# Kernel tuning notes

Hardware: AMD Instinct MI355X
Metric: run time of the kernel (lower is better)

## Reference

```python
import jax, jax.numpy as jnp
import numpy as np

B, N, F_IN, H = 16, 2048, 6, 64
NEG_INF = -jnp.inf


def setup_inputs() -> dict:
    key = jax.random.key(0)
    ks = jax.random.split(key, 16)
    x = jax.random.normal(ks[0], (B, N, F_IN), dtype=jnp.float32)
    adj = jax.random.bernoulli(ks[1], 0.5, (B, N, N)).astype(jnp.int32)
    valid = int(N * 0.9)
    mask = jnp.broadcast_to((jnp.arange(N) < valid).astype(jnp.float32)[None, :, None], (B, N, 1))
    mask = jnp.array(mask)

    def lin(k, fi, fo):
        return jax.random.normal(k, (fi, fo), dtype=jnp.float32) / np.sqrt(fi)

    return {
        'x': x, 'adj': adj, 'mask': mask,
        'W1': lin(ks[2], F_IN, H), 'a_src1': lin(ks[3], H, 1), 'a_dst1': lin(ks[4], H, 1),
        'W2': lin(ks[5], H, H), 'a_src2': lin(ks[6], H, 1), 'a_dst2': lin(ks[7], H, 1),
        'actor_w1': lin(ks[8], H, 32), 'actor_b1': jnp.zeros((32,), jnp.float32),
        'actor_w2': lin(ks[9], 32, 1), 'actor_b2': jnp.zeros((1,), jnp.float32),
        'critic_w1': lin(ks[10], H, 32), 'critic_b1': jnp.zeros((32,), jnp.float32),
        'critic_w2': lin(ks[11], 32, 1), 'critic_b2': jnp.zeros((1,), jnp.float32),
    }


def gat_layer(x, adj, mask, W, a_src, a_dst):
    h = x @ W                                    # [B,N,H]
    s = h @ a_src                                # [B,N,1]
    d = h @ a_dst                                # [B,N,1]
    e = jax.nn.leaky_relu(s + jnp.swapaxes(d, -1, -2), 0.2)   # [B,N,N]
    e = jnp.where(adj == 0, NEG_INF, e)
    e = jnp.where(jnp.swapaxes(mask, -1, -2) == 0, NEG_INF, e)
    alpha = jnp.nan_to_num(jax.nn.softmax(e, axis=-1))
    out = alpha @ h + h
    return jax.nn.elu(out) * mask


def reference(x, adj, mask, W1, a_src1, a_dst1, W2, a_src2, a_dst2,
              actor_w1, actor_b1, actor_w2, actor_b2,
              critic_w1, critic_b1, critic_w2, critic_b2):
    h = gat_layer(x, adj, mask, W1, a_src1, a_dst1)
    h = gat_layer(h, adj, mask, W2, a_src2, a_dst2)
    logits = (jax.nn.elu(h @ actor_w1 + actor_b1) @ actor_w2 + actor_b2)[..., 0]  # [B,N]
    sum_h = h.sum(axis=1)                                   # [B,H]
    valid_counts = jnp.clip(mask.sum(axis=1), 1.0)          # [B,1]
    global_h = sum_h / valid_counts
    value = (jax.nn.elu(global_h @ critic_w1 + critic_b1) @ critic_w2 + critic_b2)[..., 0]  # [B]
    return logits, value
```

## Files before the change

kernel.cpp:

```cpp
#include <hip/hip_runtime.h>
#include <hip/hip_bf16.h>

constexpr int kB = 16;
constexpr int kN = 2048;
constexpr int kH = 64;
constexpr int kF = 6;

typedef short s16x8 __attribute__((ext_vector_type(8)));
typedef float f32x4 __attribute__((ext_vector_type(4)));

__device__ __forceinline__ unsigned short f2bf(float f) {
  __hip_bfloat16 h = __float2bfloat16(f);
  unsigned short u;
  __builtin_memcpy(&u, &h, 2);
  return u;
}

__device__ __forceinline__ float bf2f(unsigned short u) {
  unsigned int b = ((unsigned int)u) << 16;
  float f;
  __builtin_memcpy(&f, &b, 4);
  return f;
}

__device__ __forceinline__ float eluf(float x) {
  return x > 0.0f ? x : __expf(x) - 1.0f;
}

__device__ __forceinline__ unsigned int pack8(uint4 a, uint4 b) {
  unsigned int t1 = (a.y << 1) + a.x;
  unsigned int t2 = (a.w << 1) + a.z;
  unsigned int n0 = (t2 << 2) + t1;
  unsigned int u1 = (b.y << 1) + b.x;
  unsigned int u2 = (b.w << 1) + b.z;
  unsigned int n1 = (u2 << 2) + u1;
  return (n1 << 4) + n0;
}

__global__ __launch_bounds__(256) void k_embed(
    const float* __restrict__ x, const float* __restrict__ W,
    const float* __restrict__ asrc, const float* __restrict__ adst,
    const float* __restrict__ mask,
    float* __restrict__ hf, unsigned short* __restrict__ hT,
    unsigned int* __restrict__ uvpk, float* __restrict__ Rr,
    float* __restrict__ sumh,
    const float* __restrict__ W2,
    unsigned short* __restrict__ w2thi, unsigned short* __restrict__ w2tlo) {
  __shared__ float lh[64][65];
  __shared__ float psd[2][4][64];
  const int r0 = blockIdx.x * 64;
  const int b = r0 >> 11;
  const int i0 = r0 & (kN - 1);
  const int t = threadIdx.x;
  const int k = t & 63;
  const int w = t >> 6;
  if (blockIdx.x == 0) {
#pragma unroll
    for (int i = 0; i < 4; ++i) sumh[t + 256 * i] = 0.0f;
  }
  if (blockIdx.x == 1) {
#pragma unroll
    for (int i = 0; i < 16; ++i) {
      const int idx = t + 256 * i;
      const int col = idx & 63, kk = idx >> 6;
      const float wv = W2[kk * kH + col];
      const unsigned short hh = f2bf(wv);
      w2thi[col * 64 + kk] = hh;
      w2tlo[col * 64 + kk] = f2bf(wv - bf2f(hh));
    }
  }
  for (int it = 0; it < 16; ++it) {
    const int rl = w * 16 + it;
    const int row = r0 + rl;
    float h = 0.0f;
#pragma unroll
    for (int f = 0; f < kF; ++f) h = fmaf(x[(size_t)row * kF + f], W[f * kH + k], h);
    lh[rl][k] = h;
    hf[(size_t)row * kH + k] = h;
  }
  __syncthreads();
  float sp = 0.0f, dp = 0.0f;
#pragma unroll
  for (int kk = 0; kk < 16; ++kk) {
    const int k2 = w * 16 + kk;
    const float hv = lh[k][k2];
    sp = fmaf(hv, asrc[k2], sp);
    dp = fmaf(hv, adst[k2], dp);
  }
  psd[0][w][k] = sp;
  psd[1][w][k] = dp;
  __syncthreads();
  if (t < 64) {
    const float s = psd[0][0][t] + psd[0][1][t] + psd[0][2][t] + psd[0][3][t];
    const float d = psd[1][0][t] + psd[1][1][t] + psd[1][2][t] + psd[1][3][t];
    const int row = r0 + t;
    const bool mv = mask[row] != 0.0f;
    const float u = mv ? __expf(d) : 0.0f;
    const float v = mv ? __expf(0.2f * d) : 0.0f;
    uvpk[row] = ((unsigned int)f2bf(u) << 16) | f2bf(v);
    Rr[row] = __expf(-0.8f * s);
  }
  const size_t tb = (size_t)b * kN * kH + (size_t)(i0 >> 5) * 2048;
  for (int it = 0; it < 16; ++it) {
    const int kk = w * 16 + it;
    hT[tb + (size_t)(k >> 5) * 2048 + kk * 32 + (k & 31)] = f2bf(lh[k][kk]);
  }
}

template <bool PACK, bool TAIL, bool EMB>
__global__ __launch_bounds__(256) void k_attn(
    const int* __restrict__ adj, unsigned int* __restrict__ bits,
    const unsigned short* __restrict__ hT,
    const unsigned int* __restrict__ uvpk, const float* __restrict__ Rr,
    const float* __restrict__ hres, const float* __restrict__ mask,
    const float* __restrict__ aw1, const float* __restrict__ ab1,
    const float* __restrict__ aw2, const float* __restrict__ ab2,
    float* __restrict__ logits, float* __restrict__ sumh,
    const unsigned short* __restrict__ w2thi, const unsigned short* __restrict__ w2tlo,
    const float* __restrict__ asrc2, const float* __restrict__ adst2,
    float* __restrict__ h2res, unsigned short* __restrict__ hT2,
    unsigned int* __restrict__ uv2, float* __restrict__ Rr2) {
  __shared__ __align__(16) char smem[32896];
  unsigned int* uvl = (unsigned int*)smem;
  unsigned int* blw = (unsigned int*)(smem + 8192);
  unsigned short* hbase = (unsigned short*)(smem + 16512);

  const int bid0 = blockIdx.x;
  const int swz = (bid0 & 7) * 128 + (bid0 >> 3);
  const int b = swz >> 6;
  const int rb = swz & 63;
  const int row0 = rb * 32;

  const int t = threadIdx.x;
  const int wv = t >> 6;
  const int l = t & 63;
  const int r = l & 15;
  const int g = l >> 4;
  const int rt = wv & 1;
  const int hf2 = wv >> 1;
  const int rloc = rt * 16 + r;

  {
    const uint4* src = (const uint4*)(uvpk + (size_t)b * kN);
    ((uint4*)uvl)[t] = src[t];
    ((uint4*)uvl)[t + 256] = src[t + 256];
  }

  const unsigned short* hTb = hT + (size_t)b * kN * kH;
  {
    *(uint4*)(hbase + 0 * 2048 + t * 8) = *(const uint4*)(hTb + t * 8);
    *(uint4*)(hbase + 1 * 2048 + t * 8) = *(const uint4*)(hTb + (size_t)32 * 2048 + t * 8);
  }
  uint4 hc0 = *(const uint4*)(hTb + (size_t)1 * 2048 + t * 8);
  uint4 hc1 = *(const uint4*)(hTb + (size_t)33 * 2048 + t * 8);
  uint4 hn0 = {}, hn1 = {};

  const int brow = t >> 3;
  const int bc = t & 7;
  const int bh = bc >> 2;
  const int bq4 = bc & 3;
  const int* adjL = adj + ((size_t)b * kN + row0 + brow) * kN + bh * 1024 + bq4 * 8;
  uint4 qcA = {}, qcB = {}, qnA = {}, qnB = {};
  if (PACK) {
    const uint4 a0 = *(const uint4*)(adjL);
    const uint4 a1 = *(const uint4*)(adjL + 4);
    ((unsigned char*)blw)[(brow * 65 + bh * 32) * 4 + bq4] = (unsigned char)pack8(a0, a1);
    qcA = *(const uint4*)(adjL + 32);
    qcB = *(const uint4*)(adjL + 36);
  } else {
#pragma unroll
    for (int ii = 0; ii < 8; ++ii) {
      const int idx = ii * 256 + t;
      const int rr2 = idx >> 6, wj = idx & 63;
      blw[rr2 * 65 + wj] = bits[((size_t)b * kN + row0 + rr2) * 64 + wj];
    }
  }

  const float Ri = Rr[(size_t)b * kN + row0 + rloc];
  __syncthreads();

  f32x4 acc0 = {0.f, 0.f, 0.f, 0.f}, acc1 = {0.f, 0.f, 0.f, 0.f};
  f32x4 acc2 = {0.f, 0.f, 0.f, 0.f}, acc3 = {0.f, 0.f, 0.f, 0.f};
  f32x4 accz = {0.f, 0.f, 0.f, 0.f};
  s16x8 ones;
#pragma unroll
  for (int e = 0; e < 8; ++e) ones[e] = (r == 0) ? (short)0x3F80 : (short)0;

  for (int jt = 0; jt < 32; ++jt) {
    if (jt < 30) {
      hn0 = *(const uint4*)(hTb + (size_t)(jt + 2) * 2048 + t * 8);
      hn1 = *(const uint4*)(hTb + (size_t)(32 + jt + 2) * 2048 + t * 8);
      if (PACK) {
        qnA = *(const uint4*)(adjL + (size_t)(jt + 2) * 32);
        qnB = *(const uint4*)(adjL + (size_t)(jt + 2) * 32 + 4);
      }
    }
    if (jt < 31) {
      const int buf = (jt + 1) & 1;
      *(uint4*)(hbase + (buf * 2 + 0) * 2048 + t * 8) = hc0;
      *(uint4*)(hbase + (buf * 2 + 1) * 2048 + t * 8) = hc1;
      if (PACK)
        ((unsigned char*)blw)[(brow * 65 + bh * 32 + jt + 1) * 4 + bq4] =
            (unsigned char)pack8(qcA, qcB);
    }

    const unsigned int bw = blw[rloc * 65 + hf2 * 32 + jt];
    const unsigned int byt = (bw >> (g * 8)) & 0xffu;
    const unsigned int* uvp = uvl + hf2 * 1024 + jt * 32 + g * 8;
    const uint4 ua = *(const uint4*)uvp;
    const uint4 ub = *(const uint4*)(uvp + 4);
    union { s16x8 v; unsigned int w[4]; } afu;
    {
      const unsigned int uvw[8] = {ua.x, ua.y, ua.z, ua.w, ub.x, ub.y, ub.z, ub.w};
#pragma unroll
      for (int p = 0; p < 4; ++p) {
        unsigned int ulb = uvw[2 * p] & 0xFFFF0000u, vlb = uvw[2 * p] << 16;
        unsigned int uhb = uvw[2 * p + 1] & 0xFFFF0000u, vhb = uvw[2 * p + 1] << 16;
        float ulf, vlf, uhf, vhf;
        __builtin_memcpy(&ulf, &ulb, 4); __builtin_memcpy(&vlf, &vlb, 4);
        __builtin_memcpy(&uhf, &uhb, 4); __builtin_memcpy(&vhf, &vhb, 4);
        const float vall = fmaxf(ulf, Ri * vlf);
        const float valh = fmaxf(uhf, Ri * vhf);
        unsigned int lbits, hbits;
        __builtin_memcpy(&lbits, &vall, 4); __builtin_memcpy(&hbits, &valh, 4);
        lbits = (byt & (1u << (2 * p))) ? lbits : 0u;
        hbits = (byt & (1u << (2 * p + 1))) ? hbits : 0u;
        afu.w[p] = (hbits & 0xFFFF0000u) | (lbits >> 16);
      }
    }
    const unsigned short* cur = hbase + ((jt & 1) * 2 + hf2) * 2048 + r * 32 + g * 8;
    const s16x8 f0 = *(const s16x8*)(cur);
    const s16x8 f1 = *(const s16x8*)(cur + 512);
    const s16x8 f2 = *(const s16x8*)(cur + 1024);
    const s16x8 f3 = *(const s16x8*)(cur + 1536);

    acc0 = __builtin_amdgcn_mfma_f32_16x16x32_bf16(afu.v, f0, acc0, 0, 0, 0);
    acc1 = __builtin_amdgcn_mfma_f32_16x16x32_bf16(afu.v, f1, acc1, 0, 0, 0);
    acc2 = __builtin_amdgcn_mfma_f32_16x16x32_bf16(afu.v, f2, acc2, 0, 0, 0);
    acc3 = __builtin_amdgcn_mfma_f32_16x16x32_bf16(afu.v, f3, acc3, 0, 0, 0);
    accz = __builtin_amdgcn_mfma_f32_16x16x32_bf16(afu.v, ones, accz, 0, 0, 0);

    asm volatile("s_waitcnt lgkmcnt(0)" ::: "memory");
    __builtin_amdgcn_s_barrier();
    hc0 = hn0; hc1 = hn1;
    if (PACK) { qcA = qnA; qcB = qnB; }
  }

  float* psumF = (float*)(smem + 16512);
  float* zsumF = (float*)(smem + 16512 + 8448);
  if (hf2 == 1) {
#pragma unroll
    for (int q = 0; q < 4; ++q) {
      const int lrow = rt * 16 + g * 4 + q;
      psumF[lrow * 66 + r + 0]  = acc0[q];
      psumF[lrow * 66 + r + 16] = acc1[q];
      psumF[lrow * 66 + r + 32] = acc2[q];
      psumF[lrow * 66 + r + 48] = acc3[q];
      if (r == 0) zsumF[lrow] = accz[q];
    }
  }
  if (PACK) {
#pragma unroll
    for (int ii = 0; ii < 8; ++ii) {
      const int idx = ii * 256 + t;
      const int rr2 = idx >> 6, wj = idx & 63;
      bits[((size_t)b * kN + row0 + rr2) * 64 + wj] = blw[rr2 * 65 + wj];
    }
  }
  __syncthreads();
  float* lhFF = (float*)smem;
  if (hf2 == 0) {
#pragma unroll
    for (int q = 0; q < 4; ++q) {
      const int lrow = rt * 16 + g * 4 + q;
      const float zq = __shfl(accz[q], (l & 48)) + zsumF[lrow];
      const float inv = (zq > 0.0f) ? 1.0f / zq : 0.0f;
      const size_t rowg = (size_t)b * kN + row0 + lrow;
      const float mk = mask[rowg];
      const float* hrp = hres + rowg * kH;
      const float o0 = eluf(fmaf(acc0[q] + psumF[lrow * 66 + r + 0],  inv, hrp[r + 0]))  * mk;
      const float o1 = eluf(fmaf(acc1[q] + psumF[lrow * 66 + r + 16], inv, hrp[r + 16])) * mk;
      const float o2 = eluf(fmaf(acc2[q] + psumF[lrow * 66 + r + 32], inv, hrp[r + 32])) * mk;
      const float o3 = eluf(fmaf(acc3[q] + psumF[lrow * 66 + r + 48], inv, hrp[r + 48])) * mk;
      lhFF[lrow * 65 + r + 0]  = o0;
      lhFF[lrow * 65 + r + 16] = o1;
      lhFF[lrow * 65 + r + 32] = o2;
      lhFF[lrow * 65 + r + 48] = o3;
    }
  }

  if (EMB) {
    __syncthreads();
    const int ntb = hf2 * 2;
    s16x8 ah[2], al[2];
    {
      const float* arow = lhFF + (rt * 16 + r) * 65;
#pragma unroll
      for (int ks = 0; ks < 2; ++ks) {
#pragma unroll
        for (int j = 0; j < 8; ++j) {
          const float v = arow[ks * 32 + g * 8 + j];
          const unsigned short hh = f2bf(v);
          ah[ks][j] = (short)hh;
          al[ks][j] = (short)f2bf(v - bf2f(hh));
        }
      }
    }
    f32x4 e0 = {0.f, 0.f, 0.f, 0.f}, e1 = {0.f, 0.f, 0.f, 0.f};
#pragma unroll
    for (int ks = 0; ks < 2; ++ks) {
      const int kof = ks * 32 + g * 8;
      {
        const s16x8 bhi = *(const s16x8*)(w2thi + (ntb * 16 + r) * 64 + kof);
        const s16x8 blo = *(const s16x8*)(w2tlo + (ntb * 16 + r) * 64 + kof);
        e0 = __builtin_amdgcn_mfma_f32_16x16x32_bf16(ah[ks], bhi, e0, 0, 0, 0);
        e0 = __builtin_amdgcn_mfma_f32_16x16x32_bf16(al[ks], bhi, e0, 0, 0, 0);
        e0 = __builtin_amdgcn_mfma_f32_16x16x32_bf16(ah[ks], blo, e0, 0, 0, 0);
      }
      {
        const s16x8 bhi = *(const s16x8*)(w2thi + ((ntb + 1) * 16 + r) * 64 + kof);
        const s16x8 blo = *(const s16x8*)(w2tlo + ((ntb + 1) * 16 + r) * 64 + kof);
        e1 = __builtin_amdgcn_mfma_f32_16x16x32_bf16(ah[ks], bhi, e1, 0, 0, 0);
        e1 = __builtin_amdgcn_mfma_f32_16x16x32_bf16(al[ks], bhi, e1, 0, 0, 0);
        e1 = __builtin_amdgcn_mfma_f32_16x16x32_bf16(ah[ks], blo, e1, 0, 0, 0);
      }
    }
    float* lh2F = (float*)(smem + 16512);
#pragma unroll
    for (int q = 0; q < 4; ++q) {
      const int lrow = rt * 16 + g * 4 + q;
      lh2F[lrow * 66 + ntb * 16 + r] = e0[q];
      lh2F[lrow * 66 + (ntb + 1) * 16 + r] = e1[q];
      const size_t rowg = (size_t)b * kN + row0 + lrow;
      h2res[rowg * kH + ntb * 16 + r] = e0[q];
      h2res[rowg * kH + (ntb + 1) * 16 + r] = e1[q];
    }
    __syncthreads();
    {
      const int kr = t & 31, wc = t >> 5;
      const size_t tb2 = (size_t)b * kN * kH + (size_t)rb * 2048;
#pragma unroll
      for (int it = 0; it < 8; ++it) {
        const int c = wc * 8 + it;
        hT2[tb2 + c * 32 + kr] = f2bf(lh2F[kr * 66 + c]);
      }
    }
    {
      const int rw = t >> 3, c0 = (t & 7) * 8;
      float sp = 0.0f, dp = 0.0f;
#pragma unroll
      for (int j = 0; j < 8; ++j) {
        const float hv = lh2F[rw * 66 + c0 + j];
        sp = fmaf(hv, asrc2[c0 + j], sp);
        dp = fmaf(hv, adst2[c0 + j], dp);
      }
#pragma unroll
      for (int o = 4; o; o >>= 1) {
        sp += __shfl_xor(sp, o);
        dp += __shfl_xor(dp, o);
      }
      if ((t & 7) == 0) {
        const size_t rowg = (size_t)b * kN + row0 + rw;
        const bool mv = mask[rowg] != 0.0f;
        const float u = mv ? __expf(dp) : 0.0f;
        const float v = mv ? __expf(0.2f * dp) : 0.0f;
        uv2[rowg] = ((unsigned int)f2bf(u) << 16) | f2bf(v);
        Rr2[rowg] = __expf(-0.8f * sp);
      }
    }
  }

  if (TAIL) {
    __syncthreads();
    const int ln = t & 31;
    const int grp = t >> 5;
#pragma unroll
    for (int rr2 = 0; rr2 < 4; ++rr2) {
      const int lrow = grp * 4 + rr2;
      float accA = ab1[ln];
#pragma unroll 8
      for (int m = 0; m < kH; ++m) accA = fmaf(lhFF[lrow * 65 + m], aw1[m * 32 + ln], accA);
      float p = eluf(accA) * aw2[ln];
#pragma unroll
      for (int o = 16; o; o >>= 1) p += __shfl_xor(p, o, 32);
      if (ln == 0) logits[(size_t)b * kN + row0 + lrow] = p + ab2[0];
    }
    float cs = 0.0f;
    const int kcol = t & 63;
    const int seg = t >> 6;
#pragma unroll
    for (int ii = 0; ii < 8; ++ii) cs += lhFF[(seg * 8 + ii) * 65 + kcol];
    float* csF = (float*)(smem + 16512 + 8704);
    csF[seg * 64 + kcol] = cs;
    __syncthreads();
    if (t < 64) atomicAdd(&sumh[b * 64 + t], csF[t] + csF[64 + t] + csF[128 + t] + csF[192 + t]);
  }
}

__global__ __launch_bounds__(64) void k_critic2(
    const float* __restrict__ sumh, const float* __restrict__ mask,
    const float* __restrict__ cw1, const float* __restrict__ cb1,
    const float* __restrict__ cw2, const float* __restrict__ cb2,
    float* __restrict__ value) {
  __shared__ float lgh[64];
  const int b = blockIdx.x, t = threadIdx.x;
  float c = 0.0f;
#pragma unroll
  for (int ii = 0; ii < 32; ++ii) c += mask[(size_t)b * kN + t + 64 * ii];
#pragma unroll
  for (int off = 32; off; off >>= 1) c += __shfl_xor(c, off);
  lgh[t] = sumh[b * 64 + t] / fmaxf(c, 1.0f);
  __syncthreads();
  if (t < 32) {
    float acc = cb1[t];
#pragma unroll 8
    for (int m = 0; m < kH; ++m) acc = fmaf(lgh[m], cw1[m * 32 + t], acc);
    float p = eluf(acc) * cw2[t];
#pragma unroll
    for (int off = 16; off; off >>= 1) p += __shfl_xor(p, off, 32);
    if (t == 0) value[b] = p + cb2[0];
  }
}

extern "C" void kernel_launch(void* const* d_in, const int* in_sizes, int n_in,
                              void* d_out, int out_size, void* d_ws, size_t ws_size,
                              hipStream_t stream) {
  const float* x = (const float*)d_in[0];
  const int* adj = (const int*)d_in[1];
  const float* mask = (const float*)d_in[2];
  const float* W1 = (const float*)d_in[3];
  const float* asrc1 = (const float*)d_in[4];
  const float* adst1 = (const float*)d_in[5];
  const float* W2 = (const float*)d_in[6];
  const float* asrc2 = (const float*)d_in[7];
  const float* adst2 = (const float*)d_in[8];
  const float* aw1 = (const float*)d_in[9];
  const float* ab1 = (const float*)d_in[10];
  const float* aw2 = (const float*)d_in[11];
  const float* ab2 = (const float*)d_in[12];
  const float* cw1 = (const float*)d_in[13];
  const float* cb1 = (const float*)d_in[14];
  const float* cw2 = (const float*)d_in[15];
  const float* cb2 = (const float*)d_in[16];
  float* logits = (float*)d_out;
  float* value = (float*)d_out + kB * kN;

  char* ws = (char*)d_ws;
  size_t off = 0;
  auto take = [&](size_t bytes) {
    char* p = ws + off;
    off = (off + bytes + 255) & ~(size_t)255;
    return p;
  };
  unsigned int* bits = (unsigned int*)take((size_t)kB * kN * (kN / 8));
  float* hA = (float*)take((size_t)kB * kN * kH * 4);
  float* hA2 = (float*)take((size_t)kB * kN * kH * 4);
  unsigned short* hT1 = (unsigned short*)take((size_t)kB * kN * kH * 2);
  unsigned short* hT2 = (unsigned short*)take((size_t)kB * kN * kH * 2);
  unsigned int* uv1 = (unsigned int*)take((size_t)kB * kN * 4);
  unsigned int* uv2 = (unsigned int*)take((size_t)kB * kN * 4);
  float* R1 = (float*)take((size_t)kB * kN * 4);
  float* R2 = (float*)take((size_t)kB * kN * 4);
  float* sumh = (float*)take(kB * kH * 4);
  unsigned short* w2thi = (unsigned short*)take(64 * 64 * 2);
  unsigned short* w2tlo = (unsigned short*)take(64 * 64 * 2);

  k_embed<<<kB * kN / 64, 256, 0, stream>>>(x, W1, asrc1, adst1, mask, hA, hT1, uv1, R1,
                                            sumh, W2, w2thi, w2tlo);
  k_attn<true, false, true><<<kB * 64, 256, 0, stream>>>(
      adj, bits, hT1, uv1, R1, hA, mask, aw1, ab1, aw2, ab2, logits, sumh,
      w2thi, w2tlo, asrc2, adst2, hA2, hT2, uv2, R2);
  k_attn<false, true, false><<<kB * 64, 256, 0, stream>>>(
      adj, bits, hT2, uv2, R2, hA2, mask, aw1, ab1, aw2, ab2, logits, sumh,
      nullptr, nullptr, nullptr, nullptr, nullptr, nullptr, nullptr, nullptr);
  k_critic2<<<kB, 64, 0, stream>>>(sumh, mask, cw1, cb1, cw2, cb2, value);
}
```

Measured before the change: 124.8 us.

## Load MFMA B-operands directly from global into registers, drop LDS staging and barriers

```diff
diff --git a/kernel.cpp b/kernel.cpp
--- a/kernel.cpp
+++ b/kernel.cpp
@@ -120,10 +120,9 @@
     const float* __restrict__ asrc2, const float* __restrict__ adst2,
     float* __restrict__ h2res, unsigned short* __restrict__ hT2,
     unsigned int* __restrict__ uv2, float* __restrict__ Rr2) {
-  __shared__ __align__(16) char smem[32896];
+  __shared__ __align__(16) char smem[26368];
   unsigned int* uvl = (unsigned int*)smem;
   unsigned int* blw = (unsigned int*)(smem + 8192);
-  unsigned short* hbase = (unsigned short*)(smem + 16512);
 
   const int bid0 = blockIdx.x;
   const int swz = (bid0 & 7) * 128 + (bid0 >> 3);
@@ -140,34 +139,26 @@
   const int hf2 = wv >> 1;
   const int rloc = rt * 16 + r;
 
+  const unsigned short* hTb = hT + (size_t)b * kN * kH;
+  const unsigned short* fbase = hTb + (size_t)hf2 * 32 * 2048 + r * 32 + g * 8;
+  uint4 fc0 = *(const uint4*)(fbase + 0);
+  uint4 fc1 = *(const uint4*)(fbase + 512);
+  uint4 fc2 = *(const uint4*)(fbase + 1024);
+  uint4 fc3 = *(const uint4*)(fbase + 1536);
+
+  const int* adjL = adj + ((size_t)b * kN + row0 + rloc) * kN + hf2 * 1024 + g * 8;
+  uint4 qc0 = {}, qc1 = {};
+  if (PACK) {
+    qc0 = *(const uint4*)(adjL);
+    qc1 = *(const uint4*)(adjL + 4);
+  }
+
   {
     const uint4* src = (const uint4*)(uvpk + (size_t)b * kN);
     ((uint4*)uvl)[t] = src[t];
     ((uint4*)uvl)[t + 256] = src[t + 256];
   }
-
-  const unsigned short* hTb = hT + (size_t)b * kN * kH;
-  {
-    *(uint4*)(hbase + 0 * 2048 + t * 8) = *(const uint4*)(hTb + t * 8);
-    *(uint4*)(hbase + 1 * 2048 + t * 8) = *(const uint4*)(hTb + (size_t)32 * 2048 + t * 8);
-  }
-  uint4 hc0 = *(const uint4*)(hTb + (size_t)1 * 2048 + t * 8);
-  uint4 hc1 = *(const uint4*)(hTb + (size_t)33 * 2048 + t * 8);
-  uint4 hn0 = {}, hn1 = {};
-
-  const int brow = t >> 3;
-  const int bc = t & 7;
-  const int bh = bc >> 2;
-  const int bq4 = bc & 3;
-  const int* adjL = adj + ((size_t)b * kN + row0 + brow) * kN + bh * 1024 + bq4 * 8;
-  uint4 qcA = {}, qcB = {}, qnA = {}, qnB = {};
-  if (PACK) {
-    const uint4 a0 = *(const uint4*)(adjL);
-    const uint4 a1 = *(const uint4*)(adjL + 4);
-    ((unsigned char*)blw)[(brow * 65 + bh * 32) * 4 + bq4] = (unsigned char)pack8(a0, a1);
-    qcA = *(const uint4*)(adjL + 32);
-    qcB = *(const uint4*)(adjL + 36);
-  } else {
+  if (!PACK) {
 #pragma unroll
     for (int ii = 0; ii < 8; ++ii) {
       const int idx = ii * 256 + t;
@@ -187,25 +178,28 @@
   for (int e = 0; e < 8; ++e) ones[e] = (r == 0) ? (short)0x3F80 : (short)0;
 
   for (int jt = 0; jt < 32; ++jt) {
-    if (jt < 30) {
-      hn0 = *(const uint4*)(hTb + (size_t)(jt + 2) * 2048 + t * 8);
-      hn1 = *(const uint4*)(hTb + (size_t)(32 + jt + 2) * 2048 + t * 8);
+    uint4 fn0, fn1, fn2, fn3;
+    uint4 qn0, qn1;
+    if (jt < 31) {
+      const unsigned short* fnb = fbase + (size_t)(jt + 1) * 2048;
+      fn0 = *(const uint4*)(fnb + 0);
+      fn1 = *(const uint4*)(fnb + 512);
+      fn2 = *(const uint4*)(fnb + 1024);
+      fn3 = *(const uint4*)(fnb + 1536);
       if (PACK) {
-        qnA = *(const uint4*)(adjL + (size_t)(jt + 2) * 32);
-        qnB = *(const uint4*)(adjL + (size_t)(jt + 2) * 32 + 4);
-      }
-    }
-    if (jt < 31) {
-      const int buf = (jt + 1) & 1;
-      *(uint4*)(hbase + (buf * 2 + 0) * 2048 + t * 8) = hc0;
-      *(uint4*)(hbase + (buf * 2 + 1) * 2048 + t * 8) = hc1;
-      if (PACK)
-        ((unsigned char*)blw)[(brow * 65 + bh * 32 + jt + 1) * 4 + bq4] =
-            (unsigned char)pack8(qcA, qcB);
-    }
-
-    const unsigned int bw = blw[rloc * 65 + hf2 * 32 + jt];
-    const unsigned int byt = (bw >> (g * 8)) & 0xffu;
+        qn0 = *(const uint4*)(adjL + (size_t)(jt + 1) * 32);
+        qn1 = *(const uint4*)(adjL + (size_t)(jt + 1) * 32 + 4);
+      }
+    }
+
+    unsigned int byt;
+    if (PACK) {
+      byt = pack8(qc0, qc1);
+      ((unsigned char*)blw)[(rloc * 65 + hf2 * 32 + jt) * 4 + g] = (unsigned char)byt;
+    } else {
+      byt = (blw[rloc * 65 + hf2 * 32 + jt] >> (g * 8)) & 0xffu;
+    }
+
     const unsigned int* uvp = uvl + hf2 * 1024 + jt * 32 + g * 8;
     const uint4 ua = *(const uint4*)uvp;
     const uint4 ub = *(const uint4*)(uvp + 4);
@@ -228,11 +222,11 @@
         afu.w[p] = (hbits & 0xFFFF0000u) | (lbits >> 16);
       }
     }
-    const unsigned short* cur = hbase + ((jt & 1) * 2 + hf2) * 2048 + r * 32 + g * 8;
-    const s16x8 f0 = *(const s16x8*)(cur);
-    const s16x8 f1 = *(const s16x8*)(cur + 512);
-    const s16x8 f2 = *(const s16x8*)(cur + 1024);
-    const s16x8 f3 = *(const s16x8*)(cur + 1536);
+
+    const s16x8 f0 = *(const s16x8*)&fc0;
+    const s16x8 f1 = *(const s16x8*)&fc1;
+    const s16x8 f2 = *(const s16x8*)&fc2;
+    const s16x8 f3 = *(const s16x8*)&fc3;
 
     acc0 = __builtin_amdgcn_mfma_f32_16x16x32_bf16(afu.v, f0, acc0, 0, 0, 0);
     acc1 = __builtin_amdgcn_mfma_f32_16x16x32_bf16(afu.v, f1, acc1, 0, 0, 0);
@@ -240,11 +234,13 @@
     acc3 = __builtin_amdgcn_mfma_f32_16x16x32_bf16(afu.v, f3, acc3, 0, 0, 0);
     accz = __builtin_amdgcn_mfma_f32_16x16x32_bf16(afu.v, ones, accz, 0, 0, 0);
 
-    asm volatile("s_waitcnt lgkmcnt(0)" ::: "memory");
-    __builtin_amdgcn_s_barrier();
-    hc0 = hn0; hc1 = hn1;
-    if (PACK) { qcA = qnA; qcB = qnB; }
-  }
+    if (jt < 31) {
+      fc0 = fn0; fc1 = fn1; fc2 = fn2; fc3 = fn3;
+      if (PACK) { qc0 = qn0; qc1 = qn1; }
+    }
+  }
+
+  __syncthreads();
 
   float* psumF = (float*)(smem + 16512);
   float* zsumF = (float*)(smem + 16512 + 8448);
```

New measurement: 146.0 us. +17.0%, slower.

## Load H fragments directly from global into registers in non-pack layer path

Applied to the files above, without the earlier changes.

```diff
diff --git a/kernel.cpp b/kernel.cpp
--- a/kernel.cpp
+++ b/kernel.cpp
@@ -35,6 +35,32 @@
   unsigned int u2 = (b.w << 1) + b.z;
   unsigned int n1 = (u2 << 2) + u1;
   return (n1 << 4) + n0;
+}
+
+__device__ __forceinline__ s16x8 make_afrag(const unsigned int* __restrict__ uvl,
+                                            int hf2, int jt, int g, float Ri,
+                                            unsigned int byt) {
+  const unsigned int* uvp = uvl + hf2 * 1024 + jt * 32 + g * 8;
+  const uint4 ua = *(const uint4*)uvp;
+  const uint4 ub = *(const uint4*)(uvp + 4);
+  union { s16x8 v; unsigned int w[4]; } afu;
+  const unsigned int uvw[8] = {ua.x, ua.y, ua.z, ua.w, ub.x, ub.y, ub.z, ub.w};
+#pragma unroll
+  for (int p = 0; p < 4; ++p) {
+    unsigned int ulb = uvw[2 * p] & 0xFFFF0000u, vlb = uvw[2 * p] << 16;
+    unsigned int uhb = uvw[2 * p + 1] & 0xFFFF0000u, vhb = uvw[2 * p + 1] << 16;
+    float ulf, vlf, uhf, vhf;
+    __builtin_memcpy(&ulf, &ulb, 4); __builtin_memcpy(&vlf, &vlb, 4);
+    __builtin_memcpy(&uhf, &uhb, 4); __builtin_memcpy(&vhf, &vhb, 4);
+    const float vall = fmaxf(ulf, Ri * vlf);
+    const float valh = fmaxf(uhf, Ri * vhf);
+    unsigned int lbits, hbits;
+    __builtin_memcpy(&lbits, &vall, 4); __builtin_memcpy(&hbits, &valh, 4);
+    lbits = (byt & (1u << (2 * p))) ? lbits : 0u;
+    hbits = (byt & (1u << (2 * p + 1))) ? hbits : 0u;
+    afu.w[p] = (hbits & 0xFFFF0000u) | (lbits >> 16);
+  }
+  return afu.v;
 }
 
 __global__ __launch_bounds__(256) void k_embed(
@@ -147,13 +173,27 @@
   }
 
   const unsigned short* hTb = hT + (size_t)b * kN * kH;
-  {
+  uint4 hc0 = {}, hc1 = {}, hn0 = {}, hn1 = {};
+  if (PACK) {
     *(uint4*)(hbase + 0 * 2048 + t * 8) = *(const uint4*)(hTb + t * 8);
     *(uint4*)(hbase + 1 * 2048 + t * 8) = *(const uint4*)(hTb + (size_t)32 * 2048 + t * 8);
-  }
-  uint4 hc0 = *(const uint4*)(hTb + (size_t)1 * 2048 + t * 8);
-  uint4 hc1 = *(const uint4*)(hTb + (size_t)33 * 2048 + t * 8);
-  uint4 hn0 = {}, hn1 = {};
+    hc0 = *(const uint4*)(hTb + (size_t)1 * 2048 + t * 8);
+    hc1 = *(const uint4*)(hTb + (size_t)33 * 2048 + t * 8);
+  }
+
+  const unsigned short* fbase = hTb + (size_t)hf2 * 32 * 2048 + r * 32 + g * 8;
+  uint4 fa0 = {}, fa1 = {}, fa2 = {}, fa3 = {};
+  uint4 fb0 = {}, fb1 = {}, fb2 = {}, fb3 = {};
+  if (!PACK) {
+    fa0 = *(const uint4*)(fbase + 0);
+    fa1 = *(const uint4*)(fbase + 512);
+    fa2 = *(const uint4*)(fbase + 1024);
+    fa3 = *(const uint4*)(fbase + 1536);
+    fb0 = *(const uint4*)(fbase + 2048 + 0);
+    fb1 = *(const uint4*)(fbase + 2048 + 512);
+    fb2 = *(const uint4*)(fbase + 2048 + 1024);
+    fb3 = *(const uint4*)(fbase + 2048 + 1536);
+  }
 
   const int brow = t >> 3;
   const int bc = t & 7;
@@ -186,64 +226,73 @@
 #pragma unroll
   for (int e = 0; e < 8; ++e) ones[e] = (r == 0) ? (short)0x3F80 : (short)0;
 
-  for (int jt = 0; jt < 32; ++jt) {
-    if (jt < 30) {
-      hn0 = *(const uint4*)(hTb + (size_t)(jt + 2) * 2048 + t * 8);
-      hn1 = *(const uint4*)(hTb + (size_t)(32 + jt + 2) * 2048 + t * 8);
-      if (PACK) {
+  if (PACK) {
+    for (int jt = 0; jt < 32; ++jt) {
+      if (jt < 30) {
+        hn0 = *(const uint4*)(hTb + (size_t)(jt + 2) * 2048 + t * 8);
+        hn1 = *(const uint4*)(hTb + (size_t)(32 + jt + 2) * 2048 + t * 8);
         qnA = *(const uint4*)(adjL + (size_t)(jt + 2) * 32);
         qnB = *(const uint4*)(adjL + (size_t)(jt + 2) * 32 + 4);
       }
-    }
-    if (jt < 31) {
-      const int buf = (jt + 1) & 1;
-      *(uint4*)(hbase + (buf * 2 + 0) * 2048 + t * 8) = hc0;
-      *(uint4*)(hbase + (buf * 2 + 1) * 2048 + t * 8) = hc1;
-      if (PACK)
+      if (jt < 31) {
+        const int buf = (jt + 1) & 1;
+        *(uint4*)(hbase + (buf * 2 + 0) * 2048 + t * 8) = hc0;
+        *(uint4*)(hbase + (buf * 2 + 1) * 2048 + t * 8) = hc1;
         ((unsigned char*)blw)[(brow * 65 + bh * 32 + jt + 1) * 4 + bq4] =
             (unsigned char)pack8(qcA, qcB);
-    }
-
-    const unsigned int bw = blw[rloc * 65 + hf2 * 32 + jt];
-    const unsigned int byt = (bw >> (g * 8)) & 0xffu;
-    const unsigned int* uvp = uvl + hf2 * 1024 + jt * 32 + g * 8;
-    const uint4 ua = *(const uint4*)uvp;
-    const uint4 ub = *(const uint4*)(uvp + 4);
-    union { s16x8 v; unsigned int w[4]; } afu;
-    {
-      const unsigned int uvw[8] = {ua.x, ua.y, ua.z, ua.w, ub.x, ub.y, ub.z, ub.w};
-#pragma unroll
-      for (int p = 0; p < 4; ++p) {
-        unsigned int ulb = uvw[2 * p] & 0xFFFF0000u, vlb = uvw[2 * p] << 16;
-        unsigned int uhb = uvw[2 * p + 1] & 0xFFFF0000u, vhb = uvw[2 * p + 1] << 16;
-        float ulf, vlf, uhf, vhf;
-        __builtin_memcpy(&ulf, &ulb, 4); __builtin_memcpy(&vlf, &vlb, 4);
-        __builtin_memcpy(&uhf, &uhb, 4); __builtin_memcpy(&vhf, &vhb, 4);
-        const float vall = fmaxf(ulf, Ri * vlf);
-        const float valh = fmaxf(uhf, Ri * vhf);
-        unsigned int lbits, hbits;
-        __builtin_memcpy(&lbits, &vall, 4); __builtin_memcpy(&hbits, &valh, 4);
-        lbits = (byt & (1u << (2 * p))) ? lbits : 0u;
-        hbits = (byt & (1u << (2 * p + 1))) ? hbits : 0u;
-        afu.w[p] = (hbits & 0xFFFF0000u) | (lbits >> 16);
-      }
-    }
-    const unsigned short* cur = hbase + ((jt & 1) * 2 + hf2) * 2048 + r * 32 + g * 8;
-    const s16x8 f0 = *(const s16x8*)(cur);
-    const s16x8 f1 = *(const s16x8*)(cur + 512);
-    const s16x8 f2 = *(const s16x8*)(cur + 1024);
-    const s16x8 f3 = *(const s16x8*)(cur + 1536);
-
-    acc0 = __builtin_amdgcn_mfma_f32_16x16x32_bf16(afu.v, f0, acc0, 0, 0, 0);
-    acc1 = __builtin_amdgcn_mfma_f32_16x16x32_bf16(afu.v, f1, acc1, 0, 0, 0);
-    acc2 = __builtin_amdgcn_mfma_f32_16x16x32_bf16(afu.v, f2, acc2, 0, 0, 0);
-    acc3 = __builtin_amdgcn_mfma_f32_16x16x32_bf16(afu.v, f3, acc3, 0, 0, 0);
-    accz = __builtin_amdgcn_mfma_f32_16x16x32_bf16(afu.v, ones, accz, 0, 0, 0);
-
-    asm volatile("s_waitcnt lgkmcnt(0)" ::: "memory");
-    __builtin_amdgcn_s_barrier();
-    hc0 = hn0; hc1 = hn1;
-    if (PACK) { qcA = qnA; qcB = qnB; }
+      }
+
+      const unsigned int bw = blw[rloc * 65 + hf2 * 32 + jt];
+      const unsigned int byt = (bw >> (g * 8)) & 0xffu;
+      const s16x8 av = make_afrag(uvl, hf2, jt, g, Ri, byt);
+
+      const unsigned short* cur = hbase + ((jt & 1) * 2 + hf2) * 2048 + r * 32 + g * 8;
+      const s16x8 f0 = *(const s16x8*)(cur);
+      const s16x8 f1 = *(const s16x8*)(cur + 512);
+      const s16x8 f2 = *(const s16x8*)(cur + 1024);
+      const s16x8 f3 = *(const s16x8*)(cur + 1536);
+
+      acc0 = __builtin_amdgcn_mfma_f32_16x16x32_bf16(av, f0, acc0, 0, 0, 0);
+      acc1 = __builtin_amdgcn_mfma_f32_16x16x32_bf16(av, f1, acc1, 0, 0, 0);
+      acc2 = __builtin_amdgcn_mfma_f32_16x16x32_bf16(av, f2, acc2, 0, 0, 0);
+      acc3 = __builtin_amdgcn_mfma_f32_16x16x32_bf16(av, f3, acc3, 0, 0, 0);
+      accz = __builtin_amdgcn_mfma_f32_16x16x32_bf16(av, ones, accz, 0, 0, 0);
+
+      asm volatile("s_waitcnt lgkmcnt(0)" ::: "memory");
+      __builtin_amdgcn_s_barrier();
+      hc0 = hn0; hc1 = hn1;
+      qcA = qnA; qcB = qnB;
+    }
+  } else {
+    for (int jt = 0; jt < 32; ++jt) {
+      uint4 fn0 = {}, fn1 = {}, fn2 = {}, fn3 = {};
+      if (jt < 30) {
+        const unsigned short* fnb = fbase + (size_t)(jt + 2) * 2048;
+        fn0 = *(const uint4*)(fnb + 0);
+        fn1 = *(const uint4*)(fnb + 512);
+        fn2 = *(const uint4*)(fnb + 1024);
+        fn3 = *(const uint4*)(fnb + 1536);
+      }
+
+      const unsigned int bw = blw[rloc * 65 + hf2 * 32 + jt];
+      const unsigned int byt = (bw >> (g * 8)) & 0xffu;
+      const s16x8 av = make_afrag(uvl, hf2, jt, g, Ri, byt);
+
+      const s16x8 f0 = *(const s16x8*)&fa0;
+      const s16x8 f1 = *(const s16x8*)&fa1;
+      const s16x8 f2 = *(const s16x8*)&fa2;
+      const s16x8 f3 = *(const s16x8*)&fa3;
+
+      acc0 = __builtin_amdgcn_mfma_f32_16x16x32_bf16(av, f0, acc0, 0, 0, 0);
+      acc1 = __builtin_amdgcn_mfma_f32_16x16x32_bf16(av, f1, acc1, 0, 0, 0);
+      acc2 = __builtin_amdgcn_mfma_f32_16x16x32_bf16(av, f2, acc2, 0, 0, 0);
+      acc3 = __builtin_amdgcn_mfma_f32_16x16x32_bf16(av, f3, acc3, 0, 0, 0);
+      accz = __builtin_amdgcn_mfma_f32_16x16x32_bf16(av, ones, accz, 0, 0, 0);
+
+      fa0 = fb0; fa1 = fb1; fa2 = fb2; fa3 = fb3;
+      fb0 = fn0; fb1 = fn1; fb2 = fn2; fb3 = fn3;
+    }
+    __syncthreads();
   }
 
   float* psumF = (float*)(smem + 16512);
```

New measurement: 130.7 us. 1.05x slower.

## Skip fully masked column tiles and row blocks in attention loop

Applied to the files above, without the earlier changes.

```diff
diff --git a/kernel.cpp b/kernel.cpp
--- a/kernel.cpp
+++ b/kernel.cpp
@@ -124,6 +124,8 @@
   unsigned int* uvl = (unsigned int*)smem;
   unsigned int* blw = (unsigned int*)(smem + 8192);
   unsigned short* hbase = (unsigned short*)(smem + 16512);
+  int* mxp = (int*)&blw[64];
+  int* rfp = (int*)&blw[129];
 
   const int bid0 = blockIdx.x;
   const int swz = (bid0 & 7) * 128 + (bid0 >> 3);
@@ -140,6 +142,8 @@
   const int hf2 = wv >> 1;
   const int rloc = rt * 16 + r;
 
+  if (t == 0) { *mxp = -1; *rfp = 0; }
+
   {
     const uint4* src = (const uint4*)(uvpk + (size_t)b * kN);
     ((uint4*)uvl)[t] = src[t];
@@ -149,24 +153,24 @@
   const unsigned short* hTb = hT + (size_t)b * kN * kH;
   {
     *(uint4*)(hbase + 0 * 2048 + t * 8) = *(const uint4*)(hTb + t * 8);
-    *(uint4*)(hbase + 1 * 2048 + t * 8) = *(const uint4*)(hTb + (size_t)32 * 2048 + t * 8);
-  }
-  uint4 hc0 = *(const uint4*)(hTb + (size_t)1 * 2048 + t * 8);
-  uint4 hc1 = *(const uint4*)(hTb + (size_t)33 * 2048 + t * 8);
+    *(uint4*)(hbase + 1 * 2048 + t * 8) = *(const uint4*)(hTb + (size_t)1 * 2048 + t * 8);
+  }
+  uint4 hc0 = *(const uint4*)(hTb + (size_t)2 * 2048 + t * 8);
+  uint4 hc1 = *(const uint4*)(hTb + (size_t)3 * 2048 + t * 8);
   uint4 hn0 = {}, hn1 = {};
 
   const int brow = t >> 3;
   const int bc = t & 7;
   const int bh = bc >> 2;
   const int bq4 = bc & 3;
-  const int* adjL = adj + ((size_t)b * kN + row0 + brow) * kN + bh * 1024 + bq4 * 8;
+  const int* adjLp = adj + ((size_t)b * kN + row0 + brow) * kN + bh * 32 + bq4 * 8;
   uint4 qcA = {}, qcB = {}, qnA = {}, qnB = {};
   if (PACK) {
-    const uint4 a0 = *(const uint4*)(adjL);
-    const uint4 a1 = *(const uint4*)(adjL + 4);
-    ((unsigned char*)blw)[(brow * 65 + bh * 32) * 4 + bq4] = (unsigned char)pack8(a0, a1);
-    qcA = *(const uint4*)(adjL + 32);
-    qcB = *(const uint4*)(adjL + 36);
+    const uint4 a0 = *(const uint4*)(adjLp);
+    const uint4 a1 = *(const uint4*)(adjLp + 4);
+    ((unsigned char*)blw)[(brow * 65 + bh) * 4 + bq4] = (unsigned char)pack8(a0, a1);
+    qcA = *(const uint4*)(adjLp + 64);
+    qcB = *(const uint4*)(adjLp + 68);
   } else {
 #pragma unroll
     for (int ii = 0; ii < 8; ++ii) {
@@ -179,6 +183,19 @@
   const float Ri = Rr[(size_t)b * kN + row0 + rloc];
   __syncthreads();
 
+  {
+    int lm = -1;
+#pragma unroll
+    for (int i = 0; i < 8; ++i)
+      if (uvl[t * 8 + i] != 0u) lm = t * 8 + i;
+    if (lm >= 0) atomicMax(mxp, lm);
+    if (t < 32 && mask[(size_t)b * kN + row0 + t] != 0.0f) atomicOr(rfp, 1);
+  }
+  __syncthreads();
+  const int mxv = *mxp;
+  const int ntj = (mxv < 0) ? 0 : ((mxv >> 6) + 1);
+  const bool ract = (*rfp != 0);
+
   f32x4 acc0 = {0.f, 0.f, 0.f, 0.f}, acc1 = {0.f, 0.f, 0.f, 0.f};
   f32x4 acc2 = {0.f, 0.f, 0.f, 0.f}, acc3 = {0.f, 0.f, 0.f, 0.f};
   f32x4 accz = {0.f, 0.f, 0.f, 0.f};
@@ -186,64 +203,66 @@
 #pragma unroll
   for (int e = 0; e < 8; ++e) ones[e] = (r == 0) ? (short)0x3F80 : (short)0;
 
-  for (int jt = 0; jt < 32; ++jt) {
-    if (jt < 30) {
-      hn0 = *(const uint4*)(hTb + (size_t)(jt + 2) * 2048 + t * 8);
-      hn1 = *(const uint4*)(hTb + (size_t)(32 + jt + 2) * 2048 + t * 8);
-      if (PACK) {
-        qnA = *(const uint4*)(adjL + (size_t)(jt + 2) * 32);
-        qnB = *(const uint4*)(adjL + (size_t)(jt + 2) * 32 + 4);
-      }
-    }
-    if (jt < 31) {
-      const int buf = (jt + 1) & 1;
-      *(uint4*)(hbase + (buf * 2 + 0) * 2048 + t * 8) = hc0;
-      *(uint4*)(hbase + (buf * 2 + 1) * 2048 + t * 8) = hc1;
-      if (PACK)
-        ((unsigned char*)blw)[(brow * 65 + bh * 32 + jt + 1) * 4 + bq4] =
-            (unsigned char)pack8(qcA, qcB);
-    }
-
-    const unsigned int bw = blw[rloc * 65 + hf2 * 32 + jt];
-    const unsigned int byt = (bw >> (g * 8)) & 0xffu;
-    const unsigned int* uvp = uvl + hf2 * 1024 + jt * 32 + g * 8;
-    const uint4 ua = *(const uint4*)uvp;
-    const uint4 ub = *(const uint4*)(uvp + 4);
-    union { s16x8 v; unsigned int w[4]; } afu;
-    {
-      const unsigned int uvw[8] = {ua.x, ua.y, ua.z, ua.w, ub.x, ub.y, ub.z, ub.w};
-#pragma unroll
-      for (int p = 0; p < 4; ++p) {
-        unsigned int ulb = uvw[2 * p] & 0xFFFF0000u, vlb = uvw[2 * p] << 16;
-        unsigned int uhb = uvw[2 * p + 1] & 0xFFFF0000u, vhb = uvw[2 * p + 1] << 16;
-        float ulf, vlf, uhf, vhf;
-        __builtin_memcpy(&ulf, &ulb, 4); __builtin_memcpy(&vlf, &vlb, 4);
-        __builtin_memcpy(&uhf, &uhb, 4); __builtin_memcpy(&vhf, &vhb, 4);
-        const float vall = fmaxf(ulf, Ri * vlf);
-        const float valh = fmaxf(uhf, Ri * vhf);
-        unsigned int lbits, hbits;
-        __builtin_memcpy(&lbits, &vall, 4); __builtin_memcpy(&hbits, &valh, 4);
-        lbits = (byt & (1u << (2 * p))) ? lbits : 0u;
-        hbits = (byt & (1u << (2 * p + 1))) ? hbits : 0u;
-        afu.w[p] = (hbits & 0xFFFF0000u) | (lbits >> 16);
-      }
-    }
-    const unsigned short* cur = hbase + ((jt & 1) * 2 + hf2) * 2048 + r * 32 + g * 8;
-    const s16x8 f0 = *(const s16x8*)(cur);
-    const s16x8 f1 = *(const s16x8*)(cur + 512);
-    const s16x8 f2 = *(const s16x8*)(cur + 1024);
-    const s16x8 f3 = *(const s16x8*)(cur + 1536);
-
-    acc0 = __builtin_amdgcn_mfma_f32_16x16x32_bf16(afu.v, f0, acc0, 0, 0, 0);
-    acc1 = __builtin_amdgcn_mfma_f32_16x16x32_bf16(afu.v, f1, acc1, 0, 0, 0);
-    acc2 = __builtin_amdgcn_mfma_f32_16x16x32_bf16(afu.v, f2, acc2, 0, 0, 0);
-    acc3 = __builtin_amdgcn_mfma_f32_16x16x32_bf16(afu.v, f3, acc3, 0, 0, 0);
-    accz = __builtin_amdgcn_mfma_f32_16x16x32_bf16(afu.v, ones, accz, 0, 0, 0);
-
-    asm volatile("s_waitcnt lgkmcnt(0)" ::: "memory");
-    __builtin_amdgcn_s_barrier();
-    hc0 = hn0; hc1 = hn1;
-    if (PACK) { qcA = qnA; qcB = qnB; }
+  if (ract) {
+    for (int jt = 0; jt < ntj; ++jt) {
+      if (jt < ntj - 2) {
+        hn0 = *(const uint4*)(hTb + (size_t)(2 * jt + 4) * 2048 + t * 8);
+        hn1 = *(const uint4*)(hTb + (size_t)(2 * jt + 5) * 2048 + t * 8);
+        if (PACK) {
+          qnA = *(const uint4*)(adjLp + (size_t)(jt + 2) * 64);
+          qnB = *(const uint4*)(adjLp + (size_t)(jt + 2) * 64 + 4);
+        }
+      }
+      if (jt < ntj - 1) {
+        const int buf = (jt + 1) & 1;
+        *(uint4*)(hbase + (buf * 2 + 0) * 2048 + t * 8) = hc0;
+        *(uint4*)(hbase + (buf * 2 + 1) * 2048 + t * 8) = hc1;
+        if (PACK)
+          ((unsigned char*)blw)[(brow * 65 + 2 * jt + 2 + bh) * 4 + bq4] =
+              (unsigned char)pack8(qcA, qcB);
+      }
+
+      const unsigned int bw = blw[rloc * 65 + 2 * jt + hf2];
+      const unsigned int byt = (bw >> (g * 8)) & 0xffu;
+      const unsigned int* uvp = uvl + (2 * jt + hf2) * 32 + g * 8;
+      const uint4 ua = *(const uint4*)uvp;
+      const uint4 ub = *(const uint4*)(uvp + 4);
+      union { s16x8 v; unsigned int w[4]; } afu;
+      {
+        const unsigned int uvw[8] = {ua.x, ua.y, ua.z, ua.w, ub.x, ub.y, ub.z, ub.w};
+#pragma unroll
+        for (int p = 0; p < 4; ++p) {
+          unsigned int ulb = uvw[2 * p] & 0xFFFF0000u, vlb = uvw[2 * p] << 16;
+          unsigned int uhb = uvw[2 * p + 1] & 0xFFFF0000u, vhb = uvw[2 * p + 1] << 16;
+          float ulf, vlf, uhf, vhf;
+          __builtin_memcpy(&ulf, &ulb, 4); __builtin_memcpy(&vlf, &vlb, 4);
+          __builtin_memcpy(&uhf, &uhb, 4); __builtin_memcpy(&vhf, &vhb, 4);
+          const float vall = fmaxf(ulf, Ri * vlf);
+          const float valh = fmaxf(uhf, Ri * vhf);
+          unsigned int lbits, hbits;
+          __builtin_memcpy(&lbits, &vall, 4); __builtin_memcpy(&hbits, &valh, 4);
+          lbits = (byt & (1u << (2 * p))) ? lbits : 0u;
+          hbits = (byt & (1u << (2 * p + 1))) ? hbits : 0u;
+          afu.w[p] = (hbits & 0xFFFF0000u) | (lbits >> 16);
+        }
+      }
+      const unsigned short* cur = hbase + ((jt & 1) * 2 + hf2) * 2048 + r * 32 + g * 8;
+      const s16x8 f0 = *(const s16x8*)(cur);
+      const s16x8 f1 = *(const s16x8*)(cur + 512);
+      const s16x8 f2 = *(const s16x8*)(cur + 1024);
+      const s16x8 f3 = *(const s16x8*)(cur + 1536);
+
+      acc0 = __builtin_amdgcn_mfma_f32_16x16x32_bf16(afu.v, f0, acc0, 0, 0, 0);
+      acc1 = __builtin_amdgcn_mfma_f32_16x16x32_bf16(afu.v, f1, acc1, 0, 0, 0);
+      acc2 = __builtin_amdgcn_mfma_f32_16x16x32_bf16(afu.v, f2, acc2, 0, 0, 0);
+      acc3 = __builtin_amdgcn_mfma_f32_16x16x32_bf16(afu.v, f3, acc3, 0, 0, 0);
+      accz = __builtin_amdgcn_mfma_f32_16x16x32_bf16(afu.v, ones, accz, 0, 0, 0);
+
+      asm volatile("s_waitcnt lgkmcnt(0)" ::: "memory");
+      __builtin_amdgcn_s_barrier();
+      hc0 = hn0; hc1 = hn1;
+      if (PACK) { qcA = qnA; qcB = qnB; }
+    }
   }
 
   float* psumF = (float*)(smem + 16512);
```

Measured after the change: 113.4 us. -9.2%, faster.
